# Kernel optimization log

Hardware: AMD Instinct MI355X
Metric: run time of the kernel (lower is better)

The kernel has to match this reference:

```python
import jax, jax.numpy as jnp
import numpy as np

B, INPUT_DIM, HEAD = 16384, 1024, 8
DIM = INPUT_DIM // HEAD


def setup_inputs() -> dict:
    key = jax.random.key(0)
    k1, k2, kw1, kb1, kw2, kw3 = jax.random.split(key, 6)
    x1 = jax.random.normal(k1, (B, INPUT_DIM), dtype=jnp.float32)
    x2 = jax.random.normal(k2, (B, INPUT_DIM), dtype=jnp.float32)
    s = 1.0 / np.sqrt(DIM)
    W1 = jax.random.uniform(kw1, (HEAD, DIM), jnp.float32, -s, s)   # per-head Linear(dim,1) weight
    b1 = jax.random.uniform(kb1, (HEAD,), jnp.float32, -s, s)       # per-head Linear(dim,1) bias
    W2 = jax.random.uniform(kw2, (HEAD, DIM), jnp.float32, -s, s)   # per-head Linear(dim,1,bias=False)
    W3 = jax.random.uniform(kw3, (HEAD, DIM, DIM), jnp.float32, -s, s)  # per-head Linear(dim,dim) [out,in]
    return {"x1": x1, "x2": x2, "W1": W1, "b1": b1, "W2": W2, "W3": W3}


def reference(x1, x2, W1, b1, W2, W3):
    b = x1.shape[0]
    h1 = x1.reshape(b, HEAD, DIM)
    h2 = x2.reshape(b, HEAD, DIM)
    # per-head scalar linears: [b, head]
    t1 = jnp.einsum('bhd,hd->bh', h1, W1) + b1
    t2 = jnp.einsum('bhd,hd->bh', h2, W2)
    # diag(w3(x1_h) @ x2_h^T) == sum((x1_h @ W3_h^T) * x2_h, -1), batched over heads
    proj = jnp.einsum('bhi,hoi->bho', h1, W3)
    t3 = jnp.sum(proj * h2, axis=-1)
    return jnp.sum(t1 + t2 + t3, axis=1)  # [b]
```

## Files before the change

kernel.cpp:

```cpp
#include <hip/hip_runtime.h>


#define NB 16384
#define NHEAD 8
#define NDIM 128

typedef __attribute__((ext_vector_type(8))) short bf16x8;
typedef __attribute__((ext_vector_type(4))) float f32x4;

__global__ __launch_bounds__(256) void prep_w3(
    const float* __restrict__ W3, short* __restrict__ whi,
    short* __restrict__ wlo)
{
    const int t    = blockIdx.x * 256 + threadIdx.x;
    const int lane = t & 63;
    const int nt   = (t >> 6) & 7;
    const int kk   = (t >> 9) & 3;
    const int h    = t >> 11;
    const int lm   = lane & 15;
    const int lg   = lane >> 4;

    const float* src = W3 + ((size_t)(h * NDIM + nt * 16 + lm)) * NDIM
                          + kk * 32 + lg * 8;
    const float4 a = *reinterpret_cast<const float4*>(src);
    const float4 b = *reinterpret_cast<const float4*>(src + 4);
    float xf[8] = {a.x, a.y, a.z, a.w, b.x, b.y, b.z, b.w};
    bf16x8 hi, lo;
#pragma unroll
    for (int j = 0; j < 8; ++j) {
        const unsigned u = __float_as_uint(xf[j]);
        hi[j] = (short)(u >> 16);
        const float hf = __uint_as_float(u & 0xffff0000u);
        lo[j] = (short)(__float_as_uint(xf[j] - hf) >> 16);
    }
    reinterpret_cast<bf16x8*>(whi)[t] = hi;
    reinterpret_cast<bf16x8*>(wlo)[t] = lo;
}

__global__ __launch_bounds__(256, 4) void bilinear_mfma(
    const float* __restrict__ x1, const float* __restrict__ x2,
    const float* __restrict__ W1, const float* __restrict__ W2,
    const short* __restrict__ whi, const short* __restrict__ wlo,
    float* __restrict__ psum)
{
    const int tid = threadIdx.x;
    const int w   = tid >> 6;
    const int l   = tid & 63;
    const int lm  = l & 15;
    const int lg  = l >> 4;
    const int h   = blockIdx.y;
    const int b0  = blockIdx.x * 64;
    const int bw  = b0 + w * 16;

    __shared__ short lhi[8][512];
    __shared__ short llo[8][512];

    const float* __restrict__ w1base = W1 + h * NDIM;
    const float* __restrict__ x1base = x1 + (size_t)(bw + lm) * (NHEAD * NDIM)
                                          + h * NDIM + lg * 8;
    const float4* __restrict__ shi = reinterpret_cast<const float4*>(
        whi + (size_t)h * 16384);
    const float4* __restrict__ slo = reinterpret_cast<const float4*>(
        wlo + (size_t)h * 16384);

    f32x4 acc[8];
#pragma unroll
    for (int nt = 0; nt < 8; ++nt) acc[nt] = (f32x4)0.f;
    float t1 = 0.f;

    float4 pa = *reinterpret_cast<const float4*>(x1base);
    float4 pb = *reinterpret_cast<const float4*>(x1base + 4);

#pragma unroll
    for (int kk = 0; kk < 4; ++kk) {
        {
            const float4 h0 = shi[kk * 512 + tid];
            const float4 h1 = shi[kk * 512 + tid + 256];
            const float4 l0 = slo[kk * 512 + tid];
            const float4 l1 = slo[kk * 512 + tid + 256];
            float4* dhi = reinterpret_cast<float4*>(&lhi[0][0]);
            float4* dlo = reinterpret_cast<float4*>(&llo[0][0]);
            dhi[tid]       = h0;
            dhi[tid + 256] = h1;
            dlo[tid]       = l0;
            dlo[tid + 256] = l1;
        }
        __syncthreads();

        const float4 ca = pa, cb = pb;
        if (kk < 3) {
            pa = *reinterpret_cast<const float4*>(x1base + (kk + 1) * 32);
            pb = *reinterpret_cast<const float4*>(x1base + (kk + 1) * 32 + 4);
        }

        bf16x8 ahi, alo;
        {
            const int k0 = kk * 32 + lg * 8;
            const float4 wa = *reinterpret_cast<const float4*>(w1base + k0);
            const float4 wb = *reinterpret_cast<const float4*>(w1base + k0 + 4);
            float xf[8]  = {ca.x, ca.y, ca.z, ca.w, cb.x, cb.y, cb.z, cb.w};
            float w1f[8] = {wa.x, wa.y, wa.z, wa.w, wb.x, wb.y, wb.z, wb.w};
#pragma unroll
            for (int j = 0; j < 8; ++j) {
                const unsigned u = __float_as_uint(xf[j]);
                ahi[j] = (short)(u >> 16);
                const float hf = __uint_as_float(u & 0xffff0000u);
                alo[j] = (short)(__float_as_uint(xf[j] - hf) >> 16);
                t1 += xf[j] * w1f[j];
            }
        }

#pragma unroll
        for (int nt = 0; nt < 8; ++nt) {
            const bf16x8 bhi = *reinterpret_cast<const bf16x8*>(&lhi[nt][l * 8]);
            const bf16x8 blo = *reinterpret_cast<const bf16x8*>(&llo[nt][l * 8]);
            acc[nt] = __builtin_amdgcn_mfma_f32_16x16x32_bf16(ahi, bhi, acc[nt], 0, 0, 0);
            acc[nt] = __builtin_amdgcn_mfma_f32_16x16x32_bf16(alo, bhi, acc[nt], 0, 0, 0);
            acc[nt] = __builtin_amdgcn_mfma_f32_16x16x32_bf16(ahi, blo, acc[nt], 0, 0, 0);
        }
        __syncthreads();
    }

    float w2v[8];
#pragma unroll
    for (int nt = 0; nt < 8; ++nt) w2v[nt] = W2[h * NDIM + nt * 16 + lm];

    float cr[4];
#pragma unroll
    for (int r = 0; r < 4; ++r) {
        const float* x2p = x2 + (size_t)(bw + lg * 4 + r) * (NHEAD * NDIM)
                            + h * NDIM + lm;
        float s = 0.f;
#pragma unroll
        for (int nt = 0; nt < 8; ++nt)
            s += (acc[nt][r] + w2v[nt]) * x2p[nt * 16];
        cr[r] = s;
    }
#pragma unroll
    for (int m = 1; m < 16; m <<= 1)
#pragma unroll
        for (int r = 0; r < 4; ++r) cr[r] += __shfl_xor(cr[r], m, 64);

    float tf = t1;
    tf += __shfl_xor(tf, 16, 64);
    tf += __shfl_xor(tf, 32, 64);
#pragma unroll
    for (int r = 0; r < 4; ++r) cr[r] += __shfl(tf, lg * 4 + r, 64);

    if (lm == 0) {
        float4 st;
        st.x = cr[0]; st.y = cr[1]; st.z = cr[2]; st.w = cr[3];
        *reinterpret_cast<float4*>(&psum[(size_t)h * NB + bw + lg * 4]) = st;
    }
}

__global__ __launch_bounds__(256) void bilinear_reduce(
    const float* __restrict__ psum, const float* __restrict__ b1,
    float* __restrict__ out)
{
    const int i = blockIdx.x * 256 + threadIdx.x;
    float bs = 0.f;
#pragma unroll
    for (int hh = 0; hh < NHEAD; ++hh) bs += b1[hh];
    float s = bs;
#pragma unroll
    for (int hh = 0; hh < NHEAD; ++hh) s += psum[(size_t)hh * NB + i];
    out[i] = s;
}

extern "C" void kernel_launch(void* const* d_in, const int* in_sizes, int n_in,
                              void* d_out, int out_size, void* d_ws, size_t ws_size,
                              hipStream_t stream) {
    const float* x1 = (const float*)d_in[0];
    const float* x2 = (const float*)d_in[1];
    const float* W1 = (const float*)d_in[2];
    const float* b1 = (const float*)d_in[3];
    const float* W2 = (const float*)d_in[4];
    const float* W3 = (const float*)d_in[5];
    float* out = (float*)d_out;

    short* whi = (short*)d_ws;
    short* wlo = whi + (size_t)NHEAD * NDIM * NDIM;
    float* psum = (float*)((char*)d_ws + 512 * 1024);

    prep_w3<<<dim3(64), dim3(256), 0, stream>>>(W3, whi, wlo);
    bilinear_mfma<<<dim3(NB / 64, NHEAD), dim3(256), 0, stream>>>(
        x1, x2, W1, W2, whi, wlo, psum);
    bilinear_reduce<<<dim3(NB / 256), dim3(256), 0, stream>>>(psum, b1, out);
}
```

Before: 36.29 us.

## Double-buffer W3 tiles in LDS and interleave heads in a 1D grid

Splits the shared-memory W3 staging into two buffers so the next k-slice's global loads are issued before the current slice's MFMAs and written to the other buffer afterwards. This removes one barrier per iteration and hides global-load latency behind compute. The grid is also flattened so that consecutive blocks cover different heads of the same batch rows, which changes how x1/x2 rows are shared in cache across blocks. LDS use per block rises from 16 KB to 32 KB, which may limit occupancy, and more registers are held live for the prefetched values.

```diff
diff --git a/kernel.cpp b/kernel.cpp
--- a/kernel.cpp
+++ b/kernel.cpp
@@ -48,45 +48,54 @@
     const int l   = tid & 63;
     const int lm  = l & 15;
     const int lg  = l >> 4;
-    const int h   = blockIdx.y;
-    const int b0  = blockIdx.x * 64;
+    const int bid = blockIdx.x;
+    const int h   = bid & 7;
+    const int b0  = (bid >> 3) * 64;
     const int bw  = b0 + w * 16;
 
-    __shared__ short lhi[8][512];
-    __shared__ short llo[8][512];
-
-    const float* __restrict__ w1base = W1 + h * NDIM;
-    const float* __restrict__ x1base = x1 + (size_t)(bw + lm) * (NHEAD * NDIM)
-                                          + h * NDIM + lg * 8;
+    __shared__ short lhi[2][4096];
+    __shared__ short llo[2][4096];
+
     const float4* __restrict__ shi = reinterpret_cast<const float4*>(
         whi + (size_t)h * 16384);
     const float4* __restrict__ slo = reinterpret_cast<const float4*>(
         wlo + (size_t)h * 16384);
 
+    const float* __restrict__ w1base = W1 + h * NDIM;
+    const float* __restrict__ x1base = x1 + (size_t)(bw + lm) * (NHEAD * NDIM)
+                                          + h * NDIM + lg * 8;
+
     f32x4 acc[8];
 #pragma unroll
     for (int nt = 0; nt < 8; ++nt) acc[nt] = (f32x4)0.f;
     float t1 = 0.f;
 
+    {
+        const float4 a0 = shi[tid];
+        const float4 a1 = shi[tid + 256];
+        const float4 c0 = slo[tid];
+        const float4 c1 = slo[tid + 256];
+        reinterpret_cast<float4*>(&lhi[0][0])[0 + tid]   = a0;
+        reinterpret_cast<float4*>(&lhi[0][0])[256 + tid] = a1;
+        reinterpret_cast<float4*>(&llo[0][0])[0 + tid]   = c0;
+        reinterpret_cast<float4*>(&llo[0][0])[256 + tid] = c1;
+    }
     float4 pa = *reinterpret_cast<const float4*>(x1base);
     float4 pb = *reinterpret_cast<const float4*>(x1base + 4);
+    __syncthreads();
 
 #pragma unroll
     for (int kk = 0; kk < 4; ++kk) {
-        {
-            const float4 h0 = shi[kk * 512 + tid];
-            const float4 h1 = shi[kk * 512 + tid + 256];
-            const float4 l0 = slo[kk * 512 + tid];
-            const float4 l1 = slo[kk * 512 + tid + 256];
-            float4* dhi = reinterpret_cast<float4*>(&lhi[0][0]);
-            float4* dlo = reinterpret_cast<float4*>(&llo[0][0]);
-            dhi[tid]       = h0;
-            dhi[tid + 256] = h1;
-            dlo[tid]       = l0;
-            dlo[tid + 256] = l1;
-        }
-        __syncthreads();
-
+        const int cur = kk & 1;
+        const int nxt = (kk + 1) & 1;
+
+        float4 nh0, nh1, nl0, nl1;
+        if (kk < 3) {
+            nh0 = shi[(kk + 1) * 512 + tid];
+            nh1 = shi[(kk + 1) * 512 + tid + 256];
+            nl0 = slo[(kk + 1) * 512 + tid];
+            nl1 = slo[(kk + 1) * 512 + tid + 256];
+        }
         const float4 ca = pa, cb = pb;
         if (kk < 3) {
             pa = *reinterpret_cast<const float4*>(x1base + (kk + 1) * 32);
@@ -112,11 +121,20 @@
 
 #pragma unroll
         for (int nt = 0; nt < 8; ++nt) {
-            const bf16x8 bhi = *reinterpret_cast<const bf16x8*>(&lhi[nt][l * 8]);
-            const bf16x8 blo = *reinterpret_cast<const bf16x8*>(&llo[nt][l * 8]);
+            const bf16x8 bhi = *reinterpret_cast<const bf16x8*>(
+                &lhi[cur][nt * 512 + l * 8]);
+            const bf16x8 blo = *reinterpret_cast<const bf16x8*>(
+                &llo[cur][nt * 512 + l * 8]);
             acc[nt] = __builtin_amdgcn_mfma_f32_16x16x32_bf16(ahi, bhi, acc[nt], 0, 0, 0);
             acc[nt] = __builtin_amdgcn_mfma_f32_16x16x32_bf16(alo, bhi, acc[nt], 0, 0, 0);
             acc[nt] = __builtin_amdgcn_mfma_f32_16x16x32_bf16(ahi, blo, acc[nt], 0, 0, 0);
+        }
+
+        if (kk < 3) {
+            reinterpret_cast<float4*>(&lhi[nxt][0])[0 + tid]   = nh0;
+            reinterpret_cast<float4*>(&lhi[nxt][0])[256 + tid] = nh1;
+            reinterpret_cast<float4*>(&llo[nxt][0])[0 + tid]   = nl0;
+            reinterpret_cast<float4*>(&llo[nxt][0])[256 + tid] = nl1;
         }
         __syncthreads();
     }
@@ -184,7 +202,7 @@
     float* psum = (float*)((char*)d_ws + 512 * 1024);
 
     prep_w3<<<dim3(64), dim3(256), 0, stream>>>(W3, whi, wlo);
-    bilinear_mfma<<<dim3(NB / 64, NHEAD), dim3(256), 0, stream>>>(
+    bilinear_mfma<<<dim3(NB / 64 * NHEAD), dim3(256), 0, stream>>>(
         x1, x2, W1, W2, whi, wlo, psum);
     bilinear_reduce<<<dim3(NB / 256), dim3(256), 0, stream>>>(psum, b1, out);
 }
```

Result: no change. 35.85 us (-1.2%).
